# Kernel optimization log

Hardware: AMD Instinct MI355X
Metric: run time of the kernel (lower is better)

The kernel has to match this reference:

```python
import jax, jax.numpy as jnp
import numpy as np


def setup_inputs() -> dict:
    key = jax.random.key(0)
    k1, k2 = jax.random.split(key)
    B, N, D = 4, 2048, 1024
    context = jax.random.normal(k1, (B, N, D), dtype=jnp.float32)
    # Dense(embedding_dim*3): kernel [D, 3D], bias [3D] (glorot-ish scale)
    W_qkv = jax.random.normal(k2, (D, 3 * D), dtype=jnp.float32) * (1.0 / np.sqrt(D))
    b_qkv = jnp.zeros((3 * D,), dtype=jnp.float32)
    return {"context": context, "W_qkv": W_qkv, "b_qkv": b_qkv}


def reference(context, W_qkv, b_qkv):
    B, N, D = context.shape
    qkv = context @ W_qkv + b_qkv                       # [B, N, 3D]
    q, k, v = jnp.split(qkv, 3, axis=-1)                # each [B, N, D]
    scores = jnp.einsum("bnd,bmd->bnm", q, k)           # [B, N, N]
    # Faithful quirk: original divides by sqrt(scores.shape[-1]) == sqrt(N)
    scores = scores / jnp.asarray(np.sqrt(N), dtype=scores.dtype)
    causal = jnp.tril(jnp.ones((N, N), dtype=jnp.float32))  # lower-triangular
    scores = jnp.where(causal == 0, -jnp.inf, scores)
    probs = jax.nn.softmax(scores, axis=-1)             # [B, N, N]
    out = jnp.einsum("bnm,bmd->bnd", probs, v)          # [B, N, D]
    return out
```

## Files before the change

kernel.cpp:

```cpp
#include <hip/hip_runtime.h>
#include <cstdint>
#include <cstddef>


typedef __attribute__((ext_vector_type(8))) __bf16 bf16x8;
typedef __attribute__((ext_vector_type(4))) float f32x4;

__device__ inline unsigned short f2bf(float f) {
  unsigned u = __float_as_uint(f);
  u = (u + 0x7FFFu + ((u >> 16) & 1u)) >> 16;
  return (unsigned short)u;
}

__device__ inline void gld16(const void* g, void* l) {
  __builtin_amdgcn_global_load_lds(
      (const __attribute__((address_space(1))) unsigned int*)g,
      (__attribute__((address_space(3))) unsigned int*)l, 16, 0, 0);
}

__device__ inline void compute_tiles(const unsigned short* As, const unsigned short* Bs,
                                     int lane, int ry, int rx, f32x4 acc[4][4]) {
#pragma unroll
  for (int kk = 0; kk < 64; kk += 32) {
    const int cbase = (kk >> 3) + (lane >> 4);
    const int csw = ((cbase ^ (lane & 7)) << 3);
    bf16x8 a[4], b[4];
#pragma unroll
    for (int mi = 0; mi < 4; mi++)
      a[mi] = *(const bf16x8*)&As[(ry + mi * 16 + (lane & 15)) * 64 + csw];
#pragma unroll
    for (int nj = 0; nj < 4; nj++)
      b[nj] = *(const bf16x8*)&Bs[(rx + nj * 16 + (lane & 15)) * 64 + csw];
#pragma unroll
    for (int mi = 0; mi < 4; mi++)
#pragma unroll
      for (int nj = 0; nj < 4; nj++)
        acc[mi][nj] = __builtin_amdgcn_mfma_f32_16x16x32_bf16(b[nj], a[mi], acc[mi][nj], 0, 0, 0);
  }
}

__device__ inline void mma_mainloop(unsigned short* As, unsigned short* Bs,
                                    const unsigned short* Abase, long strideA,
                                    const unsigned short* Bbase, long strideB,
                                    int kIters, f32x4 acc[4][4]) {
  const int lane = threadIdx.x & 63, wave = threadIdx.x >> 6;
  const int ry = (wave >> 1) * 64, rx = (wave & 1) * 64;
  const int lrow = lane >> 3;
  const int lcol = ((lane & 7) ^ lrow) * 8;
#pragma unroll
  for (int mi = 0; mi < 4; mi++)
#pragma unroll
    for (int nj = 0; nj < 4; nj++) acc[mi][nj] = (f32x4)(0.f);
  for (int kt = 0; kt < kIters; kt++) {
    const int k0 = kt * 64;
    __syncthreads();
#pragma unroll
    for (int c = 0; c < 4; c++) {
      const int q = wave * 4 + c;
      const int row = q * 8 + lrow;
      gld16(Abase + (size_t)row * strideA + k0 + lcol, &As[q * 512]);
      gld16(Bbase + (size_t)row * strideB + k0 + lcol, &Bs[q * 512]);
    }
    __syncthreads();
    compute_tiles(As, Bs, lane, ry, rx, acc);
  }
}

__device__ inline void compute_tiles64(const unsigned short* As, const unsigned short* Bs,
                                       int lane, int ry, int rx, f32x4 acc[4][2]) {
#pragma unroll
  for (int kk = 0; kk < 64; kk += 32) {
    const int cbase = (kk >> 3) + (lane >> 4);
    const int csw = ((cbase ^ (lane & 7)) << 3);
    bf16x8 a[4], b[2];
#pragma unroll
    for (int mi = 0; mi < 4; mi++)
      a[mi] = *(const bf16x8*)&As[(ry + mi * 16 + (lane & 15)) * 64 + csw];
#pragma unroll
    for (int nj = 0; nj < 2; nj++)
      b[nj] = *(const bf16x8*)&Bs[(rx + nj * 16 + (lane & 15)) * 64 + csw];
#pragma unroll
    for (int mi = 0; mi < 4; mi++)
#pragma unroll
      for (int nj = 0; nj < 2; nj++)
        acc[mi][nj] = __builtin_amdgcn_mfma_f32_16x16x32_bf16(b[nj], a[mi], acc[mi][nj], 0, 0, 0);
  }
}

__device__ inline void mma_mainloop64(unsigned short* As, unsigned short* Bs,
                                      const unsigned short* Abase, long strideA,
                                      const unsigned short* Bbase, long strideB,
                                      int kIters, f32x4 acc[4][2]) {
  const int lane = threadIdx.x & 63, wave = threadIdx.x >> 6;
  const int ry = (wave >> 1) * 64, rx = (wave & 1) * 32;
  const int lrow = lane >> 3;
  const int lcol = ((lane & 7) ^ lrow) * 8;
#pragma unroll
  for (int mi = 0; mi < 4; mi++)
#pragma unroll
    for (int nj = 0; nj < 2; nj++) acc[mi][nj] = (f32x4)(0.f);
  for (int kt = 0; kt < kIters; kt++) {
    const int k0 = kt * 64;
    __syncthreads();
#pragma unroll
    for (int c = 0; c < 4; c++) {
      const int q = wave * 4 + c;
      const int row = q * 8 + lrow;
      gld16(Abase + (size_t)row * strideA + k0 + lcol, &As[q * 512]);
    }
#pragma unroll
    for (int c = 0; c < 2; c++) {
      const int q = wave * 2 + c;
      const int row = q * 8 + lrow;
      gld16(Bbase + (size_t)row * strideB + k0 + lcol, &Bs[q * 512]);
    }
    __syncthreads();
    compute_tiles64(As, Bs, lane, ry, rx, acc);
  }
}


__global__ void k_convert(const float* __restrict__ x, unsigned short* __restrict__ y, int n4) {
  int i = blockIdx.x * blockDim.x + threadIdx.x;
  if (i >= n4) return;
  float4 v = ((const float4*)x)[i];
  ushort4 o;
  o.x = f2bf(v.x); o.y = f2bf(v.y); o.z = f2bf(v.z); o.w = f2bf(v.w);
  ((ushort4*)y)[i] = o;
}

__global__ void k_transpose_w(const float* __restrict__ W, unsigned short* __restrict__ Wt) {
  __shared__ unsigned short sm[64 * 65];
  const int n0 = blockIdx.x * 64;
  const int k0 = blockIdx.y * 64;
  for (int i = threadIdx.x; i < 4096; i += 256) {
    int r = i >> 6, c = i & 63;
    sm[c * 65 + r] = f2bf(W[(size_t)(k0 + r) * 3072 + n0 + c]);
  }
  __syncthreads();
  for (int i = threadIdx.x; i < 4096; i += 256) {
    int r = i >> 6, c = i & 63;
    Wt[(size_t)(n0 + r) * 1024 + k0 + c] = sm[r * 65 + c];
  }
}


__global__ __launch_bounds__(256) void k_gemm_qk(const unsigned short* __restrict__ A,
                                                 const unsigned short* __restrict__ Wt,
                                                 const float* __restrict__ bias,
                                                 unsigned short* __restrict__ qk) {
  __shared__ unsigned short As[128 * 64];
  __shared__ unsigned short Bs[128 * 64];
  f32x4 acc[4][4];
  const int tN0 = blockIdx.x * 128;
  const int tM0 = blockIdx.y * 128;
  mma_mainloop(As, Bs, A + (size_t)tM0 * 1024, 1024, Wt + (size_t)tN0 * 1024, 1024, 16, acc);
  const int lane = threadIdx.x & 63, wave = threadIdx.x >> 6;
  const int ry = (wave >> 1) * 64, rx = (wave & 1) * 64;
  const int l16 = lane & 15, rq = lane >> 4;
#pragma unroll
  for (int mi = 0; mi < 4; mi++) {
    const int m = tM0 + ry + mi * 16 + l16;
#pragma unroll
    for (int nj = 0; nj < 4; nj++) {
      const int n = tN0 + rx + nj * 16 + rq * 4;
      const float4 bv = *(const float4*)&bias[n];
      ushort4 o;
      o.x = f2bf(acc[mi][nj][0] + bv.x);
      o.y = f2bf(acc[mi][nj][1] + bv.y);
      o.z = f2bf(acc[mi][nj][2] + bv.z);
      o.w = f2bf(acc[mi][nj][3] + bv.w);
      *(ushort4*)&qk[(size_t)m * 2048 + n] = o;
    }
  }
}

__global__ __launch_bounds__(256) void k_gemm_v(const unsigned short* __restrict__ A,
                                                const unsigned short* __restrict__ Wt,
                                                const float* __restrict__ bias,
                                                unsigned short* __restrict__ vT) {
  __shared__ unsigned short As[128 * 64];
  __shared__ unsigned short Bs[128 * 64];
  f32x4 acc[4][4];
  const int tN0 = blockIdx.x * 128;
  const int tM0 = blockIdx.y * 128;
  mma_mainloop(As, Bs, A + (size_t)tM0 * 1024, 1024,
               Wt + (size_t)(2048 + tN0) * 1024, 1024, 16, acc);
  int tM0v = tM0;
  asm volatile("" : "+v"(tM0v));
  const int lane = threadIdx.x & 63, wave = threadIdx.x >> 6;
  const int ry = (wave >> 1) * 64, rx = (wave & 1) * 64;
  const int l16 = lane & 15, rq = lane >> 4;
#pragma unroll
  for (int mi = 0; mi < 4; mi++) {
    const int m = tM0v + ry + mi * 16 + l16;
    const int b = m >> 11, ns = m & 2047;
#pragma unroll
    for (int nj = 0; nj < 4; nj++) {
      const int d0 = tN0 + rx + nj * 16 + rq * 4;
      const float4 bv = *(const float4*)&bias[2048 + d0];
#pragma unroll
      for (int r = 0; r < 4; r++)
        vT[((size_t)(b * 1024 + d0 + r)) * 2048 + ns] =
            f2bf(acc[mi][nj][r] + ((const float*)&bv)[r]);
    }
  }
}

__global__ __launch_bounds__(256) void k_scores(const unsigned short* __restrict__ qk,
                                                unsigned short* __restrict__ P,
                                                float* __restrict__ l, float scale) {
  __shared__ unsigned short As[128 * 64];
  __shared__ unsigned short Bs[64 * 64];
  const int t = blockIdx.x, b = blockIdx.z;
  int qb = (int)((sqrtf(4.0f * (float)t + 1.0f) - 1.0f) * 0.5f);
  while (qb * (qb + 1) > t) qb--;
  while ((qb + 1) * (qb + 2) <= t) qb++;
  const int kb2 = t - qb * (qb + 1);
  f32x4 acc[4][2];
  const unsigned short* Aq = qk + ((size_t)(b * 2048 + qb * 128)) * 2048;
  const unsigned short* Bk = qk + ((size_t)(b * 2048 + kb2 * 64)) * 2048 + 1024;
  mma_mainloop64(As, Bs, Aq, 2048, Bk, 2048, 16, acc);
  const int lane = threadIdx.x & 63, wave = threadIdx.x >> 6;
  const int ry = (wave >> 1) * 64, rx = (wave & 1) * 32;
  const int l16 = lane & 15, rq = lane >> 4;
  unsigned short* Pb = P + ((size_t)(b * 2048 + qb * 128)) * 2048 + (size_t)kb2 * 64;
  float* lb = l + b * 2048 + qb * 128;
#pragma unroll
  for (int mi = 0; mi < 4; mi++) {
    const int m_local = ry + mi * 16 + l16;
    const int qi = qb * 128 + m_local;
    float rowpart = 0.f;
#pragma unroll
    for (int nj = 0; nj < 2; nj++) {
      const int n_base = rx + nj * 16 + rq * 4;
      ushort4 o;
      float p;
#pragma unroll
      for (int r = 0; r < 4; r++) {
        const int kj = kb2 * 64 + n_base + r;
        p = (kj <= qi) ? __expf(acc[mi][nj][r] * scale) : 0.f;
        rowpart += p;
        ((unsigned short*)&o)[r] = f2bf(p);
      }
      *(ushort4*)&Pb[(size_t)m_local * 2048 + n_base] = o;
    }
    rowpart += __shfl_xor(rowpart, 16, 64);
    rowpart += __shfl_xor(rowpart, 32, 64);
    if (rq == 0) atomicAdd(&lb[m_local], rowpart);
  }
}

__global__ __launch_bounds__(256) void k_pv(const unsigned short* __restrict__ P,
                                            const unsigned short* __restrict__ vT,
                                            const float* __restrict__ l,
                                            float* __restrict__ out) {
  __shared__ unsigned short As[128 * 64];
  __shared__ unsigned short Bs[64 * 64];
  const int db2 = blockIdx.x, b = blockIdx.z;
  int qb = blockIdx.y;
  if (b & 2) qb = 15 - qb;
  f32x4 acc[4][2];
  const unsigned short* Ap = P + ((size_t)(b * 2048 + qb * 128)) * 2048;
  const unsigned short* Bv = vT + ((size_t)(b * 1024 + db2 * 64)) * 2048;
  mma_mainloop64(As, Bs, Ap, 2048, Bv, 2048, (qb + 1) * 2, acc);
  const int lane = threadIdx.x & 63, wave = threadIdx.x >> 6;
  const int ry = (wave >> 1) * 64, rx = (wave & 1) * 32;
  const int l16 = lane & 15, rq = lane >> 4;
  const float* lb = l + b * 2048 + qb * 128;
  float* ob = out + ((size_t)(b * 2048 + qb * 128)) * 1024 + db2 * 64;
#pragma unroll
  for (int mi = 0; mi < 4; mi++) {
    const int m_local = ry + mi * 16 + l16;
    const float inv = 1.0f / lb[m_local];
#pragma unroll
    for (int nj = 0; nj < 2; nj++) {
      const int n_base = rx + nj * 16 + rq * 4;
      float4 o;
      o.x = acc[mi][nj][0] * inv;
      o.y = acc[mi][nj][1] * inv;
      o.z = acc[mi][nj][2] * inv;
      o.w = acc[mi][nj][3] * inv;
      *(float4*)&ob[(size_t)m_local * 1024 + n_base] = o;
    }
  }
}


extern "C" void kernel_launch(void* const* d_in, const int* in_sizes, int n_in,
                              void* d_out, int out_size, void* d_ws, size_t ws_size,
                              hipStream_t stream) {
  const float* ctx  = (const float*)d_in[0];
  const float* W    = (const float*)d_in[1];
  const float* bias = (const float*)d_in[2];
  float* out = (float*)d_out;

  char* ws = (char*)d_ws;
  unsigned short* Actx = (unsigned short*)(ws + 0);
  unsigned short* Wt   = (unsigned short*)(ws + 16777216);
  unsigned short* qk   = (unsigned short*)(ws + 23068672);
  unsigned short* vT   = (unsigned short*)(ws + 56623104);
  unsigned short* P    = (unsigned short*)(ws + 73400320);
  float*          lsum = (float*)(ws + 106954752);

  hipMemsetAsync(lsum, 0, 4 * 2048 * sizeof(float), stream);
  k_convert<<<8192, 256, 0, stream>>>(ctx, Actx, (8192 * 1024) / 4);
  k_transpose_w<<<dim3(48, 16), 256, 0, stream>>>(W, Wt);
  k_gemm_qk<<<dim3(16, 64), 256, 0, stream>>>(Actx, Wt, bias, qk);
  k_gemm_v<<<dim3(8, 64), 256, 0, stream>>>(Actx, Wt, bias, vT);
  k_scores<<<dim3(272, 1, 4), 256, 0, stream>>>(qk, P, lsum, 0.022097086912079608f);
  k_pv<<<dim3(16, 16, 4), 256, 0, stream>>>(P, vT, lsum, out);
}
```

Measured before the change: 254.0 us.

## Fuse QK and V projection GEMMs into one pipelined 256x256 double-buffered kernel

Replaces the two separate 128x128 projection GEMMs with one kernel using 256x256 tiles, 8 waves and double-buffered LDS. Global-to-LDS loads for the next k-step are issued in quarter stages interleaved with MFMA quads, using explicit vmcnt waits, barriers and setprio. A block-index swizzle is added for L2 locality. This targets load latency and synchronization stalls in the QKV projection, at the cost of higher register and LDS pressure and tight hand-scheduled correctness.

New measurement: 251.2 us. Within noise of the previous version (-1.1%).

```diff
diff --git a/kernel.cpp b/kernel.cpp
--- a/kernel.cpp
+++ b/kernel.cpp
@@ -18,51 +18,190 @@
       (__attribute__((address_space(3))) unsigned int*)l, 16, 0, 0);
 }
 
-__device__ inline void compute_tiles(const unsigned short* As, const unsigned short* Bs,
-                                     int lane, int ry, int rx, f32x4 acc[4][4]) {
-#pragma unroll
-  for (int kk = 0; kk < 64; kk += 32) {
-    const int cbase = (kk >> 3) + (lane >> 4);
-    const int csw = ((cbase ^ (lane & 7)) << 3);
-    bf16x8 a[4], b[4];
+
+__device__ inline void stage_Ahalf(const unsigned short* Agb, int k0,
+                                   unsigned short* Abuf, int half,
+                                   int wave, int lrow, int lcol) {
+#pragma unroll
+  for (int i = 0; i < 2; i++) {
+    const int c = wave * 2 + i;
+    const int rg = ((c >> 3) << 7) + ((c & 7) << 3) + (half << 6);
+    gld16(Agb + (size_t)(rg + lrow) * 1024 + k0 + lcol, Abuf + rg * 64);
+  }
+}
+
+__device__ inline void stage_Bhalf(const unsigned short* Bgb, int k0,
+                                   unsigned short* Bbuf, int half,
+                                   int wave, int lrow, int lcol) {
+#pragma unroll
+  for (int i = 0; i < 2; i++) {
+    const int c = wave * 2 + i;
+    const int rg = ((c >> 2) << 6) + ((c & 3) << 3) + (half << 5);
+    gld16(Bgb + (size_t)(rg + lrow) * 1024 + k0 + lcol, Bbuf + rg * 64);
+  }
+}
+
+__device__ inline void read_Ahalf(const unsigned short* buf, int wm, int half,
+                                  int lane, bf16x8 (&a)[4][2]) {
+#pragma unroll
+  for (int ks = 0; ks < 2; ks++) {
+    const int csw = ((((ks << 2) + (lane >> 4)) ^ (lane & 7)) << 3);
+#pragma unroll
+    for (int mi = 0; mi < 4; mi++) {
+      const int R = wm * 128 + half * 64 + mi * 16 + (lane & 15);
+      a[mi][ks] = *(const bf16x8*)&buf[R * 64 + csw];
+    }
+  }
+}
+
+__device__ inline void read_Bhalf(const unsigned short* buf, int wn, int half,
+                                  int lane, bf16x8 (&b)[2][2]) {
+#pragma unroll
+  for (int ks = 0; ks < 2; ks++) {
+    const int csw = ((((ks << 2) + (lane >> 4)) ^ (lane & 7)) << 3);
+#pragma unroll
+    for (int nj = 0; nj < 2; nj++) {
+      const int R = wn * 64 + half * 32 + nj * 16 + (lane & 15);
+      b[nj][ks] = *(const bf16x8*)&buf[R * 64 + csw];
+    }
+  }
+}
+
+__device__ inline void mma_quad(const bf16x8 (&a)[4][2], const bf16x8 (&b)[2][2],
+                                f32x4 (&acc)[8][4], const int ah, const int bh) {
+#pragma unroll
+  for (int ks = 0; ks < 2; ks++)
 #pragma unroll
     for (int mi = 0; mi < 4; mi++)
-      a[mi] = *(const bf16x8*)&As[(ry + mi * 16 + (lane & 15)) * 64 + csw];
-#pragma unroll
-    for (int nj = 0; nj < 4; nj++)
-      b[nj] = *(const bf16x8*)&Bs[(rx + nj * 16 + (lane & 15)) * 64 + csw];
-#pragma unroll
-    for (int mi = 0; mi < 4; mi++)
-#pragma unroll
-      for (int nj = 0; nj < 4; nj++)
-        acc[mi][nj] = __builtin_amdgcn_mfma_f32_16x16x32_bf16(b[nj], a[mi], acc[mi][nj], 0, 0, 0);
-  }
-}
-
-__device__ inline void mma_mainloop(unsigned short* As, unsigned short* Bs,
-                                    const unsigned short* Abase, long strideA,
-                                    const unsigned short* Bbase, long strideB,
-                                    int kIters, f32x4 acc[4][4]) {
-  const int lane = threadIdx.x & 63, wave = threadIdx.x >> 6;
-  const int ry = (wave >> 1) * 64, rx = (wave & 1) * 64;
+#pragma unroll
+      for (int nj = 0; nj < 2; nj++)
+        acc[ah * 4 + mi][bh * 2 + nj] = __builtin_amdgcn_mfma_f32_16x16x32_bf16(
+            b[nj][ks], a[mi][ks], acc[ah * 4 + mi][bh * 2 + nj], 0, 0, 0);
+}
+
+#define QKV_FENCE()                         \
+  __builtin_amdgcn_s_barrier();             \
+  asm volatile("" ::: "memory");            \
+  __builtin_amdgcn_sched_barrier(0)
+
+template <bool STAGE, int V0, int V1, int V2>
+__device__ inline void qkv_tile(const unsigned short* Agb, const unsigned short* Bgb,
+                                int k0n, const unsigned short* Ar, const unsigned short* Br,
+                                unsigned short* Aw, unsigned short* Bw,
+                                int wave, int lane, int wm, int wn,
+                                f32x4 (&acc)[8][4]) {
   const int lrow = lane >> 3;
   const int lcol = ((lane & 7) ^ lrow) * 8;
-#pragma unroll
-  for (int mi = 0; mi < 4; mi++)
+  bf16x8 aLo[4][2], aHi[4][2], bLo[2][2], bHi[2][2];
+  if (STAGE) stage_Ahalf(Agb, k0n, Aw, 0, wave, lrow, lcol);
+  asm volatile("s_waitcnt vmcnt(%0)" ::"i"(V0) : "memory");
+  QKV_FENCE();
+  read_Ahalf(Ar, wm, 0, lane, aLo);
+  read_Bhalf(Br, wn, 0, lane, bLo);
+  __builtin_amdgcn_s_setprio(1);
+  mma_quad(aLo, bLo, acc, 0, 0);
+  __builtin_amdgcn_s_setprio(0);
+  __builtin_amdgcn_sched_barrier(0);
+  __builtin_amdgcn_s_barrier();
+  if (STAGE) stage_Bhalf(Bgb, k0n, Bw, 0, wave, lrow, lcol);
+  asm volatile("s_waitcnt vmcnt(%0)" ::"i"(V1) : "memory");
+  QKV_FENCE();
+  read_Bhalf(Br, wn, 1, lane, bHi);
+  __builtin_amdgcn_s_setprio(1);
+  mma_quad(aLo, bHi, acc, 0, 1);
+  __builtin_amdgcn_s_setprio(0);
+  __builtin_amdgcn_sched_barrier(0);
+  __builtin_amdgcn_s_barrier();
+  if (STAGE) stage_Bhalf(Bgb, k0n, Bw, 1, wave, lrow, lcol);
+  asm volatile("s_waitcnt vmcnt(%0)" ::"i"(V2) : "memory");
+  QKV_FENCE();
+  read_Ahalf(Ar, wm, 1, lane, aHi);
+  __builtin_amdgcn_s_setprio(1);
+  mma_quad(aHi, bHi, acc, 1, 1);
+  __builtin_amdgcn_s_setprio(0);
+  __builtin_amdgcn_sched_barrier(0);
+  __builtin_amdgcn_s_barrier();
+  if (STAGE) stage_Ahalf(Agb, k0n, Aw, 1, wave, lrow, lcol);
+  __builtin_amdgcn_s_setprio(1);
+  mma_quad(aHi, bLo, acc, 1, 0);
+  __builtin_amdgcn_s_setprio(0);
+  __builtin_amdgcn_sched_barrier(0);
+  __builtin_amdgcn_s_barrier();
+}
+
+__global__ __launch_bounds__(512, 2) void k_gemm_qkv(
+    const unsigned short* __restrict__ A, const unsigned short* __restrict__ Wt,
+    const float* __restrict__ bias, unsigned short* __restrict__ qk,
+    unsigned short* __restrict__ vT) {
+  __shared__ unsigned short sA[2 * 16384];
+  __shared__ unsigned short sB[2 * 16384];
+  const int bid = blockIdx.y * 12 + blockIdx.x;
+  const int swz = (bid & 7) * 48 + (bid >> 3);
+  const int nb = swz % 12, mb = swz / 12;
+  const int tN0 = nb * 256, tM0 = mb * 256;
+  const unsigned short* Agb = A + (size_t)tM0 * 1024;
+  const unsigned short* Bgb = Wt + (size_t)tN0 * 1024;
+  const int lane = threadIdx.x & 63, wave = threadIdx.x >> 6;
+  const int wm = wave >> 2, wn = wave & 3;
+  const int lrow = lane >> 3, lcol = ((lane & 7) ^ lrow) * 8;
+
+  f32x4 acc[8][4];
+#pragma unroll
+  for (int mi = 0; mi < 8; mi++)
 #pragma unroll
     for (int nj = 0; nj < 4; nj++) acc[mi][nj] = (f32x4)(0.f);
-  for (int kt = 0; kt < kIters; kt++) {
-    const int k0 = kt * 64;
-    __syncthreads();
-#pragma unroll
-    for (int c = 0; c < 4; c++) {
-      const int q = wave * 4 + c;
-      const int row = q * 8 + lrow;
-      gld16(Abase + (size_t)row * strideA + k0 + lcol, &As[q * 512]);
-      gld16(Bbase + (size_t)row * strideB + k0 + lcol, &Bs[q * 512]);
-    }
-    __syncthreads();
-    compute_tiles(As, Bs, lane, ry, rx, acc);
+
+  stage_Ahalf(Agb, 0, sA, 0, wave, lrow, lcol);
+  stage_Bhalf(Bgb, 0, sB, 0, wave, lrow, lcol);
+  stage_Bhalf(Bgb, 0, sB, 1, wave, lrow, lcol);
+  stage_Ahalf(Agb, 0, sA, 1, wave, lrow, lcol);
+
+  for (int kt = 0; kt < 15; kt++) {
+    const unsigned short* Ar = sA + (kt & 1) * 16384;
+    const unsigned short* Br = sB + (kt & 1) * 16384;
+    unsigned short* Aw = sA + ((kt + 1) & 1) * 16384;
+    unsigned short* Bw = sB + ((kt + 1) & 1) * 16384;
+    qkv_tile<true, 6, 6, 6>(Agb, Bgb, (kt + 1) * 64, Ar, Br, Aw, Bw,
+                            wave, lane, wm, wn, acc);
+  }
+  qkv_tile<false, 4, 2, 0>(Agb, Bgb, 0, sA + 16384, sB + 16384, sA, sB,
+                           wave, lane, wm, wn, acc);
+
+  const int l16 = lane & 15, rq = lane >> 4;
+  int m0 = tM0 + wm * 128;
+  asm volatile("" : "+v"(m0));
+  if (tN0 < 2048) {
+#pragma unroll
+    for (int mi = 0; mi < 8; mi++) {
+      const int m = m0 + mi * 16 + l16;
+#pragma unroll
+      for (int nj = 0; nj < 4; nj++) {
+        const int n = tN0 + wn * 64 + nj * 16 + rq * 4;
+        const float4 bv = *(const float4*)&bias[n];
+        ushort4 o;
+        o.x = f2bf(acc[mi][nj][0] + bv.x);
+        o.y = f2bf(acc[mi][nj][1] + bv.y);
+        o.z = f2bf(acc[mi][nj][2] + bv.z);
+        o.w = f2bf(acc[mi][nj][3] + bv.w);
+        *(ushort4*)&qk[(size_t)m * 2048 + n] = o;
+      }
+    }
+  } else {
+    const int d0b = tN0 - 2048 + wn * 64;
+#pragma unroll
+    for (int mi = 0; mi < 8; mi++) {
+      const int m = m0 + mi * 16 + l16;
+      const int b = m >> 11, ns = m & 2047;
+#pragma unroll
+      for (int nj = 0; nj < 4; nj++) {
+        const int d0 = d0b + nj * 16 + rq * 4;
+        const float4 bv = *(const float4*)&bias[2048 + d0];
+#pragma unroll
+        for (int r = 0; r < 4; r++)
+          vT[((size_t)(b * 1024 + d0 + r)) * 2048 + ns] =
+              f2bf(acc[mi][nj][r] + ((const float*)&bv)[r]);
+      }
+    }
   }
 }
 
@@ -144,68 +283,6 @@
   }
 }
 
-
-__global__ __launch_bounds__(256) void k_gemm_qk(const unsigned short* __restrict__ A,
-                                                 const unsigned short* __restrict__ Wt,
-                                                 const float* __restrict__ bias,
-                                                 unsigned short* __restrict__ qk) {
-  __shared__ unsigned short As[128 * 64];
-  __shared__ unsigned short Bs[128 * 64];
-  f32x4 acc[4][4];
-  const int tN0 = blockIdx.x * 128;
-  const int tM0 = blockIdx.y * 128;
-  mma_mainloop(As, Bs, A + (size_t)tM0 * 1024, 1024, Wt + (size_t)tN0 * 1024, 1024, 16, acc);
-  const int lane = threadIdx.x & 63, wave = threadIdx.x >> 6;
-  const int ry = (wave >> 1) * 64, rx = (wave & 1) * 64;
-  const int l16 = lane & 15, rq = lane >> 4;
-#pragma unroll
-  for (int mi = 0; mi < 4; mi++) {
-    const int m = tM0 + ry + mi * 16 + l16;
-#pragma unroll
-    for (int nj = 0; nj < 4; nj++) {
-      const int n = tN0 + rx + nj * 16 + rq * 4;
-      const float4 bv = *(const float4*)&bias[n];
-      ushort4 o;
-      o.x = f2bf(acc[mi][nj][0] + bv.x);
-      o.y = f2bf(acc[mi][nj][1] + bv.y);
-      o.z = f2bf(acc[mi][nj][2] + bv.z);
-      o.w = f2bf(acc[mi][nj][3] + bv.w);
-      *(ushort4*)&qk[(size_t)m * 2048 + n] = o;
-    }
-  }
-}
-
-__global__ __launch_bounds__(256) void k_gemm_v(const unsigned short* __restrict__ A,
-                                                const unsigned short* __restrict__ Wt,
-                                                const float* __restrict__ bias,
-                                                unsigned short* __restrict__ vT) {
-  __shared__ unsigned short As[128 * 64];
-  __shared__ unsigned short Bs[128 * 64];
-  f32x4 acc[4][4];
-  const int tN0 = blockIdx.x * 128;
-  const int tM0 = blockIdx.y * 128;
-  mma_mainloop(As, Bs, A + (size_t)tM0 * 1024, 1024,
-               Wt + (size_t)(2048 + tN0) * 1024, 1024, 16, acc);
-  int tM0v = tM0;
-  asm volatile("" : "+v"(tM0v));
-  const int lane = threadIdx.x & 63, wave = threadIdx.x >> 6;
-  const int ry = (wave >> 1) * 64, rx = (wave & 1) * 64;
-  const int l16 = lane & 15, rq = lane >> 4;
-#pragma unroll
-  for (int mi = 0; mi < 4; mi++) {
-    const int m = tM0v + ry + mi * 16 + l16;
-    const int b = m >> 11, ns = m & 2047;
-#pragma unroll
-    for (int nj = 0; nj < 4; nj++) {
-      const int d0 = tN0 + rx + nj * 16 + rq * 4;
-      const float4 bv = *(const float4*)&bias[2048 + d0];
-#pragma unroll
-      for (int r = 0; r < 4; r++)
-        vT[((size_t)(b * 1024 + d0 + r)) * 2048 + ns] =
-            f2bf(acc[mi][nj][r] + ((const float*)&bv)[r]);
-    }
-  }
-}
 
 __global__ __launch_bounds__(256) void k_scores(const unsigned short* __restrict__ qk,
                                                 unsigned short* __restrict__ P,
@@ -306,8 +383,7 @@
   hipMemsetAsync(lsum, 0, 4 * 2048 * sizeof(float), stream);
   k_convert<<<8192, 256, 0, stream>>>(ctx, Actx, (8192 * 1024) / 4);
   k_transpose_w<<<dim3(48, 16), 256, 0, stream>>>(W, Wt);
-  k_gemm_qk<<<dim3(16, 64), 256, 0, stream>>>(Actx, Wt, bias, qk);
-  k_gemm_v<<<dim3(8, 64), 256, 0, stream>>>(Actx, Wt, bias, vT);
+  k_gemm_qkv<<<dim3(12, 32), 512, 0, stream>>>(Actx, Wt, bias, qk, vT);
   k_scores<<<dim3(272, 1, 4), 256, 0, stream>>>(qk, P, lsum, 0.022097086912079608f);
   k_pv<<<dim3(16, 16, 4), 256, 0, stream>>>(P, vT, lsum, out);
 }
```

## Enlarge attention score and PV tiles to 256x64 per block

Applied to the files above, without the earlier changes.

Raises the query-row tile of the scores and PV kernels from 128 to 256 rows. Each wave now computes 64x64 instead of 64x32, which improves MFMA-to-load reuse and halves the number of blocks. The causal block indexing is remapped to match. The cost is fewer blocks, and therefore less parallelism and coarser load balance on the causal triangle, plus more LDS and register use per block.

After: 261.1 us. +2.8%, slower.

```diff
diff --git a/kernel.cpp b/kernel.cpp
--- a/kernel.cpp
+++ b/kernel.cpp
@@ -66,45 +66,24 @@
   }
 }
 
-__device__ inline void compute_tiles64(const unsigned short* As, const unsigned short* Bs,
-                                       int lane, int ry, int rx, f32x4 acc[4][2]) {
-#pragma unroll
-  for (int kk = 0; kk < 64; kk += 32) {
-    const int cbase = (kk >> 3) + (lane >> 4);
-    const int csw = ((cbase ^ (lane & 7)) << 3);
-    bf16x8 a[4], b[2];
-#pragma unroll
-    for (int mi = 0; mi < 4; mi++)
-      a[mi] = *(const bf16x8*)&As[(ry + mi * 16 + (lane & 15)) * 64 + csw];
-#pragma unroll
-    for (int nj = 0; nj < 2; nj++)
-      b[nj] = *(const bf16x8*)&Bs[(rx + nj * 16 + (lane & 15)) * 64 + csw];
-#pragma unroll
-    for (int mi = 0; mi < 4; mi++)
-#pragma unroll
-      for (int nj = 0; nj < 2; nj++)
-        acc[mi][nj] = __builtin_amdgcn_mfma_f32_16x16x32_bf16(b[nj], a[mi], acc[mi][nj], 0, 0, 0);
-  }
-}
-
-__device__ inline void mma_mainloop64(unsigned short* As, unsigned short* Bs,
-                                      const unsigned short* Abase, long strideA,
-                                      const unsigned short* Bbase, long strideB,
-                                      int kIters, f32x4 acc[4][2]) {
-  const int lane = threadIdx.x & 63, wave = threadIdx.x >> 6;
-  const int ry = (wave >> 1) * 64, rx = (wave & 1) * 32;
+__device__ inline void mma_mainloop256(unsigned short* As, unsigned short* Bs,
+                                       const unsigned short* Abase, long strideA,
+                                       const unsigned short* Bbase, long strideB,
+                                       int kIters, f32x4 acc[4][4]) {
+  const int lane = threadIdx.x & 63, wave = threadIdx.x >> 6;
+  const int ry = wave * 64;
   const int lrow = lane >> 3;
   const int lcol = ((lane & 7) ^ lrow) * 8;
 #pragma unroll
   for (int mi = 0; mi < 4; mi++)
 #pragma unroll
-    for (int nj = 0; nj < 2; nj++) acc[mi][nj] = (f32x4)(0.f);
+    for (int nj = 0; nj < 4; nj++) acc[mi][nj] = (f32x4)(0.f);
   for (int kt = 0; kt < kIters; kt++) {
     const int k0 = kt * 64;
     __syncthreads();
 #pragma unroll
-    for (int c = 0; c < 4; c++) {
-      const int q = wave * 4 + c;
+    for (int c = 0; c < 8; c++) {
+      const int q = wave * 8 + c;
       const int row = q * 8 + lrow;
       gld16(Abase + (size_t)row * strideA + k0 + lcol, &As[q * 512]);
     }
@@ -115,7 +94,7 @@
       gld16(Bbase + (size_t)row * strideB + k0 + lcol, &Bs[q * 512]);
     }
     __syncthreads();
-    compute_tiles64(As, Bs, lane, ry, rx, acc);
+    compute_tiles(As, Bs, lane, ry, 0, acc);
   }
 }
 
@@ -207,38 +186,39 @@
   }
 }
 
+
 __global__ __launch_bounds__(256) void k_scores(const unsigned short* __restrict__ qk,
                                                 unsigned short* __restrict__ P,
                                                 float* __restrict__ l, float scale) {
-  __shared__ unsigned short As[128 * 64];
+  __shared__ unsigned short As[256 * 64];
   __shared__ unsigned short Bs[64 * 64];
   const int t = blockIdx.x, b = blockIdx.z;
-  int qb = (int)((sqrtf(4.0f * (float)t + 1.0f) - 1.0f) * 0.5f);
-  while (qb * (qb + 1) > t) qb--;
-  while ((qb + 1) * (qb + 2) <= t) qb++;
-  const int kb2 = t - qb * (qb + 1);
-  f32x4 acc[4][2];
-  const unsigned short* Aq = qk + ((size_t)(b * 2048 + qb * 128)) * 2048;
-  const unsigned short* Bk = qk + ((size_t)(b * 2048 + kb2 * 64)) * 2048 + 1024;
-  mma_mainloop64(As, Bs, Aq, 2048, Bk, 2048, 16, acc);
-  const int lane = threadIdx.x & 63, wave = threadIdx.x >> 6;
-  const int ry = (wave >> 1) * 64, rx = (wave & 1) * 32;
-  const int l16 = lane & 15, rq = lane >> 4;
-  unsigned short* Pb = P + ((size_t)(b * 2048 + qb * 128)) * 2048 + (size_t)kb2 * 64;
-  float* lb = l + b * 2048 + qb * 128;
+  int qb = (int)((sqrtf(2.0f * (float)t + 1.0f) - 1.0f) * 0.5f);
+  while (2 * qb * (qb + 1) > t) qb--;
+  while (2 * (qb + 1) * (qb + 2) <= t) qb++;
+  const int kb = t - 2 * qb * (qb + 1);
+  f32x4 acc[4][4];
+  const unsigned short* Aq = qk + ((size_t)(b * 2048 + qb * 256)) * 2048;
+  const unsigned short* Bk = qk + ((size_t)(b * 2048 + kb * 64)) * 2048 + 1024;
+  mma_mainloop256(As, Bs, Aq, 2048, Bk, 2048, 16, acc);
+  const int lane = threadIdx.x & 63, wave = threadIdx.x >> 6;
+  const int ry = wave * 64;
+  const int l16 = lane & 15, rq = lane >> 4;
+  unsigned short* Pb = P + ((size_t)(b * 2048 + qb * 256)) * 2048 + (size_t)kb * 64;
+  float* lb = l + b * 2048 + qb * 256;
 #pragma unroll
   for (int mi = 0; mi < 4; mi++) {
     const int m_local = ry + mi * 16 + l16;
-    const int qi = qb * 128 + m_local;
+    const int qi = qb * 256 + m_local;
     float rowpart = 0.f;
 #pragma unroll
-    for (int nj = 0; nj < 2; nj++) {
-      const int n_base = rx + nj * 16 + rq * 4;
+    for (int nj = 0; nj < 4; nj++) {
+      const int n_base = nj * 16 + rq * 4;
       ushort4 o;
       float p;
 #pragma unroll
       for (int r = 0; r < 4; r++) {
-        const int kj = kb2 * 64 + n_base + r;
+        const int kj = kb * 64 + n_base + r;
         p = (kj <= qi) ? __expf(acc[mi][nj][r] * scale) : 0.f;
         rowpart += p;
         ((unsigned short*)&o)[r] = f2bf(p);
@@ -255,27 +235,27 @@
                                             const unsigned short* __restrict__ vT,
                                             const float* __restrict__ l,
                                             float* __restrict__ out) {
-  __shared__ unsigned short As[128 * 64];
+  __shared__ unsigned short As[256 * 64];
   __shared__ unsigned short Bs[64 * 64];
   const int db2 = blockIdx.x, b = blockIdx.z;
   int qb = blockIdx.y;
-  if (b & 2) qb = 15 - qb;
-  f32x4 acc[4][2];
-  const unsigned short* Ap = P + ((size_t)(b * 2048 + qb * 128)) * 2048;
+  if (b & 2) qb = 7 - qb;
+  f32x4 acc[4][4];
+  const unsigned short* Ap = P + ((size_t)(b * 2048 + qb * 256)) * 2048;
   const unsigned short* Bv = vT + ((size_t)(b * 1024 + db2 * 64)) * 2048;
-  mma_mainloop64(As, Bs, Ap, 2048, Bv, 2048, (qb + 1) * 2, acc);
-  const int lane = threadIdx.x & 63, wave = threadIdx.x >> 6;
-  const int ry = (wave >> 1) * 64, rx = (wave & 1) * 32;
-  const int l16 = lane & 15, rq = lane >> 4;
-  const float* lb = l + b * 2048 + qb * 128;
-  float* ob = out + ((size_t)(b * 2048 + qb * 128)) * 1024 + db2 * 64;
+  mma_mainloop256(As, Bs, Ap, 2048, Bv, 2048, (qb + 1) * 4, acc);
+  const int lane = threadIdx.x & 63, wave = threadIdx.x >> 6;
+  const int ry = wave * 64;
+  const int l16 = lane & 15, rq = lane >> 4;
+  const float* lb = l + b * 2048 + qb * 256;
+  float* ob = out + ((size_t)(b * 2048 + qb * 256)) * 1024 + db2 * 64;
 #pragma unroll
   for (int mi = 0; mi < 4; mi++) {
     const int m_local = ry + mi * 16 + l16;
     const float inv = 1.0f / lb[m_local];
 #pragma unroll
-    for (int nj = 0; nj < 2; nj++) {
-      const int n_base = rx + nj * 16 + rq * 4;
+    for (int nj = 0; nj < 4; nj++) {
+      const int n_base = nj * 16 + rq * 4;
       float4 o;
       o.x = acc[mi][nj][0] * inv;
       o.y = acc[mi][nj][1] * inv;
@@ -308,6 +288,6 @@
   k_transpose_w<<<dim3(48, 16), 256, 0, stream>>>(W, Wt);
   k_gemm_qk<<<dim3(16, 64), 256, 0, stream>>>(Actx, Wt, bias, qk);
   k_gemm_v<<<dim3(8, 64), 256, 0, stream>>>(Actx, Wt, bias, vT);
-  k_scores<<<dim3(272, 1, 4), 256, 0, stream>>>(qk, P, lsum, 0.022097086912079608f);
-  k_pv<<<dim3(16, 16, 4), 256, 0, stream>>>(P, vT, lsum, out);
-}
+  k_scores<<<dim3(144, 1, 4), 256, 0, stream>>>(qk, P, lsum, 0.022097086912079608f);
+  k_pv<<<dim3(16, 8, 4), 256, 0, stream>>>(P, vT, lsum, out);
+}
```

## Merge prep kernels, split QK GEMM launch, reorder PV blocks longest-first

Applied to the files above, without the earlier changes.

Combines the context conversion and weight transpose into a single launch to remove one kernel launch gap. The QK projection GEMM is split into two launches over halves of the rows, which adds a launch and changes nothing else in the work. The PV kernel uses a 1D grid that schedules the heaviest (largest causal extent) query blocks first across all batches and feature tiles, meant to reduce the tail imbalance. Splitting the GEMM adds launch overhead with no clear benefit.

After: 242.8 us. -4.4%, faster.

```diff
diff --git a/kernel.cpp b/kernel.cpp
--- a/kernel.cpp
+++ b/kernel.cpp
@@ -119,28 +119,29 @@
   }
 }
 
-
-__global__ void k_convert(const float* __restrict__ x, unsigned short* __restrict__ y, int n4) {
-  int i = blockIdx.x * blockDim.x + threadIdx.x;
-  if (i >= n4) return;
-  float4 v = ((const float4*)x)[i];
-  ushort4 o;
-  o.x = f2bf(v.x); o.y = f2bf(v.y); o.z = f2bf(v.z); o.w = f2bf(v.w);
-  ((ushort4*)y)[i] = o;
-}
-
-__global__ void k_transpose_w(const float* __restrict__ W, unsigned short* __restrict__ Wt) {
+__global__ void k_prep(const float* __restrict__ x, unsigned short* __restrict__ y,
+                       const float* __restrict__ W, unsigned short* __restrict__ Wt) {
   __shared__ unsigned short sm[64 * 65];
-  const int n0 = blockIdx.x * 64;
-  const int k0 = blockIdx.y * 64;
-  for (int i = threadIdx.x; i < 4096; i += 256) {
-    int r = i >> 6, c = i & 63;
-    sm[c * 65 + r] = f2bf(W[(size_t)(k0 + r) * 3072 + n0 + c]);
-  }
-  __syncthreads();
-  for (int i = threadIdx.x; i < 4096; i += 256) {
-    int r = i >> 6, c = i & 63;
-    Wt[(size_t)(n0 + r) * 1024 + k0 + c] = sm[r * 65 + c];
+  const int bid = blockIdx.x;
+  if (bid < 8192) {
+    const int i = bid * 256 + threadIdx.x;
+    float4 v = ((const float4*)x)[i];
+    ushort4 o;
+    o.x = f2bf(v.x); o.y = f2bf(v.y); o.z = f2bf(v.z); o.w = f2bf(v.w);
+    ((ushort4*)y)[i] = o;
+  } else {
+    const int t = bid - 8192;
+    const int n0 = (t % 48) * 64;
+    const int k0 = (t / 48) * 64;
+    for (int i = threadIdx.x; i < 4096; i += 256) {
+      int r = i >> 6, c = i & 63;
+      sm[c * 65 + r] = f2bf(W[(size_t)(k0 + r) * 3072 + n0 + c]);
+    }
+    __syncthreads();
+    for (int i = threadIdx.x; i < 4096; i += 256) {
+      int r = i >> 6, c = i & 63;
+      Wt[(size_t)(n0 + r) * 1024 + k0 + c] = sm[r * 65 + c];
+    }
   }
 }
 
@@ -148,12 +149,13 @@
 __global__ __launch_bounds__(256) void k_gemm_qk(const unsigned short* __restrict__ A,
                                                  const unsigned short* __restrict__ Wt,
                                                  const float* __restrict__ bias,
-                                                 unsigned short* __restrict__ qk) {
+                                                 unsigned short* __restrict__ qk,
+                                                 int mbase) {
   __shared__ unsigned short As[128 * 64];
   __shared__ unsigned short Bs[128 * 64];
   f32x4 acc[4][4];
   const int tN0 = blockIdx.x * 128;
-  const int tM0 = blockIdx.y * 128;
+  const int tM0 = mbase + blockIdx.y * 128;
   mma_mainloop(As, Bs, A + (size_t)tM0 * 1024, 1024, Wt + (size_t)tN0 * 1024, 1024, 16, acc);
   const int lane = threadIdx.x & 63, wave = threadIdx.x >> 6;
   const int ry = (wave >> 1) * 64, rx = (wave & 1) * 64;
@@ -206,6 +208,7 @@
     }
   }
 }
+
 
 __global__ __launch_bounds__(256) void k_scores(const unsigned short* __restrict__ qk,
                                                 unsigned short* __restrict__ P,
@@ -257,9 +260,11 @@
                                             float* __restrict__ out) {
   __shared__ unsigned short As[128 * 64];
   __shared__ unsigned short Bs[64 * 64];
-  const int db2 = blockIdx.x, b = blockIdx.z;
-  int qb = blockIdx.y;
-  if (b & 2) qb = 15 - qb;
+  const int t = blockIdx.x;
+  const int qb = 15 - (t >> 6);
+  const int r = t & 63;
+  const int db2 = r >> 2;
+  const int b = r & 3;
   f32x4 acc[4][2];
   const unsigned short* Ap = P + ((size_t)(b * 2048 + qb * 128)) * 2048;
   const unsigned short* Bv = vT + ((size_t)(b * 1024 + db2 * 64)) * 2048;
@@ -304,10 +309,10 @@
   float*          lsum = (float*)(ws + 106954752);
 
   hipMemsetAsync(lsum, 0, 4 * 2048 * sizeof(float), stream);
-  k_convert<<<8192, 256, 0, stream>>>(ctx, Actx, (8192 * 1024) / 4);
-  k_transpose_w<<<dim3(48, 16), 256, 0, stream>>>(W, Wt);
-  k_gemm_qk<<<dim3(16, 64), 256, 0, stream>>>(Actx, Wt, bias, qk);
+  k_prep<<<8960, 256, 0, stream>>>(ctx, Actx, W, Wt);
+  k_gemm_qk<<<dim3(16, 32), 256, 0, stream>>>(Actx, Wt, bias, qk, 0);
+  k_gemm_qk<<<dim3(16, 32), 256, 0, stream>>>(Actx, Wt, bias, qk, 4096);
   k_gemm_v<<<dim3(8, 64), 256, 0, stream>>>(Actx, Wt, bias, vT);
   k_scores<<<dim3(272, 1, 4), 256, 0, stream>>>(qk, P, lsum, 0.022097086912079608f);
-  k_pv<<<dim3(16, 16, 4), 256, 0, stream>>>(P, vT, lsum, out);
-}
+  k_pv<<<1024, 256, 0, stream>>>(P, vT, lsum, out);
+}
```
